# Kernel tuning notes

Measured on AMD Instinct MI355X. Metric: run time of the kernel, lower is better.

Reference implementation:

```python
import jax, jax.numpy as jnp
import numpy as np


def setup_inputs() -> dict:
    key = jax.random.key(0)
    # Uniform in (0.9, 1.1) so the running product over 8192 elements stays finite.
    x = jax.random.uniform(key, (4096, 8192), dtype=jnp.float32, minval=0.9, maxval=1.1)
    return {"x": x}


def reference(x) -> jnp.ndarray:
    # Inclusive prefix product along dim 1 (matches cumprod_dim1_cuda / torch.cumprod(x, dim=1)).
    return jnp.cumprod(x, axis=1)
```

## Files before the change

### kernel.cpp

```cpp
#include <hip/hip_runtime.h>


#define N      8192
#define T      256
#define CHUNK  32
#define PADN   (N + (N / 32))

__device__ __forceinline__ int pidx(int e) { return e + (e >> 5); }

__global__ __launch_bounds__(T) void cumprod_rows_kernel(
    const float* __restrict__ x, float* __restrict__ out, int n_rows)
{
    __shared__ float lds[PADN];
    __shared__ float wsum[T / 64];

    const int row = blockIdx.x;
    if (row >= n_rows) return;
    const int tid = threadIdx.x;

    const float* __restrict__ xr   = x   + (size_t)row * N;
    float*       __restrict__ outr = out + (size_t)row * N;

#pragma unroll
    for (int v = 0; v < N / (T * 4); ++v) {
        const int e  = (v * T + tid) * 4;
        const float4 d = *reinterpret_cast<const float4*>(xr + e);
        const int pe = pidx(e);
        lds[pe + 0] = d.x; lds[pe + 1] = d.y;
        lds[pe + 2] = d.z; lds[pe + 3] = d.w;
    }
    __syncthreads();

    const int pbase = tid * (CHUNK + 1);
    float vals[CHUNK];
    float p = 1.0f;
#pragma unroll
    for (int j = 0; j < CHUNK; ++j) {
        p *= lds[pbase + j];
        vals[j] = p;
    }

    const int lane = tid & 63;
    const int wid  = tid >> 6;

    float inc = p;
#pragma unroll
    for (int off = 1; off < 64; off <<= 1) {
        const float o = __shfl_up(inc, off, 64);
        if (lane >= off) inc *= o;
    }
    if (lane == 63) wsum[wid] = inc;
    __syncthreads();

    float wpre = 1.0f;
    for (int w = 0; w < wid; ++w) wpre *= wsum[w];

    float excl = __shfl_up(inc, 1, 64);
    if (lane == 0) excl = 1.0f;
    excl *= wpre;

#pragma unroll
    for (int j = 0; j < CHUNK; ++j) lds[pbase + j] = vals[j] * excl;
    __syncthreads();

#pragma unroll
    for (int v = 0; v < N / (T * 4); ++v) {
        const int e  = (v * T + tid) * 4;
        const int pe = pidx(e);
        float4 d;
        d.x = lds[pe + 0]; d.y = lds[pe + 1];
        d.z = lds[pe + 2]; d.w = lds[pe + 3];
        *reinterpret_cast<float4*>(outr + e) = d;
    }
}

extern "C" void kernel_launch(void* const* d_in, const int* in_sizes, int n_in,
                              void* d_out, int out_size, void* d_ws, size_t ws_size,
                              hipStream_t stream)
{
    const float* x   = (const float*)d_in[0];
    float*       out = (float*)d_out;
    const int n_rows = in_sizes[0] / N;
    cumprod_rows_kernel<<<n_rows, T, 0, stream>>>(x, out, n_rows);
}
```

Baseline: 227.8 us.

## Load contiguous per-thread chunks directly from global, dropping LDS staging

Each thread now reads its 32 contiguous elements straight from global memory into registers with float4 loads and writes results back the same way. This removes the LDS transpose buffer and two block barriers. The cost is that global accesses become strided across lanes, with each thread touching a separate 128-byte segment, so coalescing drops and memory efficiency may suffer.

```diff
diff --git a/kernel.cpp b/kernel.cpp
--- a/kernel.cpp
+++ b/kernel.cpp
@@ -4,44 +4,33 @@
 #define N      8192
 #define T      256
 #define CHUNK  32
-#define PADN   (N + (N / 32))
-
-__device__ __forceinline__ int pidx(int e) { return e + (e >> 5); }
 
 __global__ __launch_bounds__(T) void cumprod_rows_kernel(
     const float* __restrict__ x, float* __restrict__ out, int n_rows)
 {
-    __shared__ float lds[PADN];
-    __shared__ float wsum[T / 64];
+    __shared__ float wtot[T / 64];
 
     const int row = blockIdx.x;
     if (row >= n_rows) return;
-    const int tid = threadIdx.x;
+    const int tid  = threadIdx.x;
+    const int lane = tid & 63;
+    const int wid  = tid >> 6;
 
-    const float* __restrict__ xr   = x   + (size_t)row * N;
-    float*       __restrict__ outr = out + (size_t)row * N;
+    const float* __restrict__ xr   = x   + (size_t)row * N + (size_t)tid * CHUNK;
+    float*       __restrict__ outr = out + (size_t)row * N + (size_t)tid * CHUNK;
 
+    float vals[CHUNK];
+    const float4* __restrict__ src = reinterpret_cast<const float4*>(xr);
 #pragma unroll
-    for (int v = 0; v < N / (T * 4); ++v) {
-        const int e  = (v * T + tid) * 4;
-        const float4 d = *reinterpret_cast<const float4*>(xr + e);
-        const int pe = pidx(e);
-        lds[pe + 0] = d.x; lds[pe + 1] = d.y;
-        lds[pe + 2] = d.z; lds[pe + 3] = d.w;
+    for (int i = 0; i < CHUNK / 4; ++i) {
+        const float4 d = src[i];
+        vals[4 * i + 0] = d.x; vals[4 * i + 1] = d.y;
+        vals[4 * i + 2] = d.z; vals[4 * i + 3] = d.w;
     }
-    __syncthreads();
 
-    const int pbase = tid * (CHUNK + 1);
-    float vals[CHUNK];
     float p = 1.0f;
 #pragma unroll
-    for (int j = 0; j < CHUNK; ++j) {
-        p *= lds[pbase + j];
-        vals[j] = p;
-    }
-
-    const int lane = tid & 63;
-    const int wid  = tid >> 6;
+    for (int j = 0; j < CHUNK; ++j) { p *= vals[j]; vals[j] = p; }
 
     float inc = p;
 #pragma unroll
@@ -49,28 +38,22 @@
         const float o = __shfl_up(inc, off, 64);
         if (lane >= off) inc *= o;
     }
-    if (lane == 63) wsum[wid] = inc;
+    if (lane == 63) wtot[wid] = inc;
     __syncthreads();
-
-    float wpre = 1.0f;
-    for (int w = 0; w < wid; ++w) wpre *= wsum[w];
 
     float excl = __shfl_up(inc, 1, 64);
     if (lane == 0) excl = 1.0f;
-    excl *= wpre;
+#pragma unroll
+    for (int w = 0; w < T / 64; ++w)
+        if (w < wid) excl *= wtot[w];
 
+    float4* __restrict__ dst = reinterpret_cast<float4*>(outr);
 #pragma unroll
-    for (int j = 0; j < CHUNK; ++j) lds[pbase + j] = vals[j] * excl;
-    __syncthreads();
-
-#pragma unroll
-    for (int v = 0; v < N / (T * 4); ++v) {
-        const int e  = (v * T + tid) * 4;
-        const int pe = pidx(e);
+    for (int i = 0; i < CHUNK / 4; ++i) {
         float4 d;
-        d.x = lds[pe + 0]; d.y = lds[pe + 1];
-        d.z = lds[pe + 2]; d.w = lds[pe + 3];
-        *reinterpret_cast<float4*>(outr + e) = d;
+        d.x = vals[4 * i + 0] * excl; d.y = vals[4 * i + 1] * excl;
+        d.z = vals[4 * i + 2] * excl; d.w = vals[4 * i + 3] * excl;
+        dst[i] = d;
     }
 }
 
```

Result: slower. 238.1 us (+4.5%).
